# Performance work log

Measured on AMD Instinct MI355X. Metric: run time of the kernel, lower is better.

## Reference

```python
import jax, jax.numpy as jnp
import numpy as np

B, N, DIN, DOUT = 8, 2048, 512, 512
EDGE_P = 0.01  # edge probability for the random binary adjacency


def setup_inputs() -> dict:
    key = jax.random.key(0)
    k1, k2, k3, k4 = jax.random.split(key, 4)
    inputs = jax.random.normal(k1, (B, N, DIN), dtype=jnp.float32)
    # binary dense adjacency (dense_to_sparse discards weights -> edges are adj != 0)
    adj = (jax.random.uniform(k2, (B, N, N)) < EDGE_P).astype(jnp.float32)
    W = jax.random.normal(k3, (DIN, DOUT), dtype=jnp.float32) / np.sqrt(DIN)
    b = jax.random.normal(k4, (DOUT,), dtype=jnp.float32) * 0.01
    return {"inputs": inputs, "adj": adj, "W": W, "b": b}


def _gcn_norm(adj):
    # binary edge mask (edge weights from dense_to_sparse are discarded)
    A = (adj != 0).astype(adj.dtype)
    # add remaining self-loops: force diagonal to 1
    eye = jnp.eye(A.shape[-1], dtype=A.dtype)
    A = jnp.maximum(A, eye)
    deg = A.sum(axis=-1)                       # [B, N]
    dinv = jnp.where(deg > 0, jax.lax.rsqrt(deg), 0.0)
    # D^-1/2 (A + I) D^-1/2
    return dinv[..., :, None] * A * dinv[..., None, :]


def reference(inputs, adj, W, b):
    norm = _gcn_norm(adj)                      # [B, N, N]
    h = jnp.einsum('bnf,fo->bno', inputs, W)   # linear (no internal bias)
    agg = jnp.einsum('bnm,bmo->bno', norm, h)  # degree-normalized aggregation
    return jnp.tanh(agg + b)
```

## Files before the change

### kernel.cpp

```cpp
#include <hip/hip_runtime.h>
#include <hip/hip_bf16.h>
#include <math.h>


#define NROWS 16384
#define NCOLS 2048
#define DF    512
#define CAP   64

typedef __attribute__((ext_vector_type(8))) short bf16x8;
typedef __attribute__((ext_vector_type(4))) float f32x4;

typedef const void __attribute__((address_space(1))) gvoid_t;
typedef void __attribute__((address_space(3))) svoid_t;

__global__ __launch_bounds__(256) void convert_kernel(
    const float* __restrict__ X, const float* __restrict__ W,
    __hip_bfloat16* __restrict__ Xb, __hip_bfloat16* __restrict__ WT) {
  __shared__ float t[64][65];
  const int bid = blockIdx.x;
  const int tid = threadIdx.x;
  if (bid < 8192) {
    const int idx = bid * 256 + tid;
    const float4 v = ((const float4*)X)[idx];
    union { ushort4 u; __hip_bfloat16 h[4]; } p;
    p.h[0] = __float2bfloat16(v.x);
    p.h[1] = __float2bfloat16(v.y);
    p.h[2] = __float2bfloat16(v.z);
    p.h[3] = __float2bfloat16(v.w);
    ((ushort4*)Xb)[idx] = p.u;
  } else {
    const int b2 = bid - 8192;
    const int bx = b2 & 7, by = b2 >> 3;
    const int tx = tid & 63, ty = tid >> 6;
    #pragma unroll
    for (int i = 0; i < 16; ++i)
      t[ty + i * 4][tx] = W[(size_t)(by * 64 + ty + i * 4) * DF + bx * 64 + tx];
    __syncthreads();
    #pragma unroll
    for (int i = 0; i < 16; ++i)
      WT[(size_t)(bx * 64 + ty + i * 4) * DF + by * 64 + tx] =
          __float2bfloat16(t[tx][ty + i * 4]);
  }
}

__global__ __launch_bounds__(256) void build_edges(
    const float* __restrict__ adj, int* __restrict__ cnt,
    int* __restrict__ edges, float* __restrict__ dinv) {
  const int wave = threadIdx.x >> 6;
  const int lane = threadIdx.x & 63;
  const int r = blockIdx.x * 4 + wave;
  const int n = r & (NCOLS - 1);
  const float4* row4 = (const float4*)(adj + (size_t)r * NCOLS);
  const unsigned long long lt = (1ull << lane) - 1ull;
  int base = 0;
  for (int k = 0; k < NCOLS / 256; ++k) {
    const float4 v = row4[k * 64 + lane];
    const int c0 = k * 256 + lane * 4;
    const bool f0 = (v.x != 0.0f) || (c0 + 0 == n);
    const bool f1 = (v.y != 0.0f) || (c0 + 1 == n);
    const bool f2 = (v.z != 0.0f) || (c0 + 2 == n);
    const bool f3 = (v.w != 0.0f) || (c0 + 3 == n);
    const unsigned long long m0 = __ballot(f0);
    const unsigned long long m1 = __ballot(f1);
    const unsigned long long m2 = __ballot(f2);
    const unsigned long long m3 = __ballot(f3);
    const int n0 = __popcll(m0), n1 = __popcll(m1), n2 = __popcll(m2), n3 = __popcll(m3);
    if (f0) { int p = base + __popcll(m0 & lt);                 if (p < CAP) edges[(size_t)r * CAP + p] = c0 + 0; }
    if (f1) { int p = base + n0 + __popcll(m1 & lt);            if (p < CAP) edges[(size_t)r * CAP + p] = c0 + 1; }
    if (f2) { int p = base + n0 + n1 + __popcll(m2 & lt);       if (p < CAP) edges[(size_t)r * CAP + p] = c0 + 2; }
    if (f3) { int p = base + n0 + n1 + n2 + __popcll(m3 & lt);  if (p < CAP) edges[(size_t)r * CAP + p] = c0 + 3; }
    base += n0 + n1 + n2 + n3;
  }
  if (lane == 0) {
    cnt[r] = base < CAP ? base : CAP;
    dinv[r] = rsqrtf((float)base);
  }
}

__global__ __launch_bounds__(256) void gemm_bf16(
    const __hip_bfloat16* __restrict__ A, const __hip_bfloat16* __restrict__ BT,
    __hip_bfloat16* __restrict__ H) {
  __shared__ __hip_bfloat16 As[128 * 32];
  __shared__ __hip_bfloat16 Bs[128 * 32];
  const int tid = threadIdx.x;
  const int lane = tid & 63;
  const int w = tid >> 6;
  const int bm = blockIdx.y * 128;
  const int bn = blockIdx.x * 128;
  const int wm = (w >> 1) * 64;
  const int wn = (w & 1) * 64;

  f32x4 acc[4][4] = {};

  const int srow = tid >> 2;
  const int scol = (tid & 3) * 8;
  const int kl = (lane >> 4) * 8;
  const int rl = lane & 15;

  for (int k0 = 0; k0 < DF; k0 += 32) {
    #pragma unroll
    for (int i = 0; i < 2; ++i) {
      const __hip_bfloat16* ga = A + (size_t)(bm + i * 64 + srow) * DF + k0 + scol;
      const __hip_bfloat16* gb = BT + (size_t)(bn + i * 64 + srow) * DF + k0 + scol;
      char* la = (char*)As + i * 4096 + w * 1024;
      char* lb = (char*)Bs + i * 4096 + w * 1024;
      __builtin_amdgcn_global_load_lds((gvoid_t*)ga, (svoid_t*)la, 16, 0, 0);
      __builtin_amdgcn_global_load_lds((gvoid_t*)gb, (svoid_t*)lb, 16, 0, 0);
    }
    __syncthreads();

    bf16x8 af[4], bf[4];
    #pragma unroll
    for (int mi = 0; mi < 4; ++mi)
      af[mi] = *(const bf16x8*)&As[(wm + mi * 16 + rl) * 32 + kl];
    #pragma unroll
    for (int ni = 0; ni < 4; ++ni)
      bf[ni] = *(const bf16x8*)&Bs[(wn + ni * 16 + rl) * 32 + kl];
    #pragma unroll
    for (int mi = 0; mi < 4; ++mi)
      #pragma unroll
      for (int ni = 0; ni < 4; ++ni)
        acc[mi][ni] = __builtin_amdgcn_mfma_f32_16x16x32_bf16(af[mi], bf[ni], acc[mi][ni], 0, 0, 0);
    __syncthreads();
  }

  const int rq = (lane >> 4) * 4;
  #pragma unroll
  for (int mi = 0; mi < 4; ++mi)
    #pragma unroll
    for (int ni = 0; ni < 4; ++ni) {
      const int col = bn + wn + ni * 16 + rl;
      #pragma unroll
      for (int j = 0; j < 4; ++j) {
        const int row = bm + wm + mi * 16 + rq + j;
        H[(size_t)row * DF + col] = __float2bfloat16(acc[mi][ni][j]);
      }
    }
}

__global__ __launch_bounds__(256) void aggregate(
    const __hip_bfloat16* __restrict__ h, const int* __restrict__ cnt,
    const int* __restrict__ edges, const float* __restrict__ dinv,
    const float* __restrict__ bias, float* __restrict__ out) {
  __shared__ int   eL[CAP];
  __shared__ float wL[CAP];
  const int j = blockIdx.x;
  const int r = (j & 7) * NCOLS + (j >> 3);
  const int b = r >> 11;
  const int tid = threadIdx.x;
  const int c = cnt[r];
  if (tid < c) {
    const int m = edges[(size_t)r * CAP + tid];
    eL[tid] = m;
    wL[tid] = dinv[(b << 11) + m];
  }
  __syncthreads();

  float ax = 0.0f, ay = 0.0f;
  for (int e = 0; e < c; ++e) {
    const int m = eL[e];
    const float wgt = wL[e];
    const unsigned hv = *(const unsigned*)&h[((size_t)(b << 11) + m) * DF + tid * 2];
    ax += wgt * __uint_as_float(hv << 16);
    ay += wgt * __uint_as_float(hv & 0xffff0000u);
  }
  const float dn = dinv[r];
  const float2 bv = *(const float2*)&bias[tid * 2];
  float2 o;
  o.x = tanhf(ax * dn + bv.x);
  o.y = tanhf(ay * dn + bv.y);
  *(float2*)&out[(size_t)r * DF + tid * 2] = o;
}

extern "C" void kernel_launch(void* const* d_in, const int* in_sizes, int n_in,
                              void* d_out, int out_size, void* d_ws, size_t ws_size,
                              hipStream_t stream) {
  const float* X    = (const float*)d_in[0];
  const float* adj  = (const float*)d_in[1];
  const float* W    = (const float*)d_in[2];
  const float* bias = (const float*)d_in[3];
  float* out = (float*)d_out;

  char* ws = (char*)d_ws;
  __hip_bfloat16* Xb   = (__hip_bfloat16*)(ws);
  __hip_bfloat16* WT   = (__hip_bfloat16*)(ws + 16777216);
  __hip_bfloat16* h    = (__hip_bfloat16*)(ws + 17301504);
  float*          dinv = (float*)(ws + 34078720);
  int*            cnt  = (int*)  (ws + 34144256);
  int*            edges= (int*)  (ws + 34209792);

  convert_kernel<<<8256, 256, 0, stream>>>(X, W, Xb, WT);
  build_edges<<<NROWS / 4, 256, 0, stream>>>(adj, cnt, edges, dinv);
  gemm_bf16<<<dim3(4, 128), 256, 0, stream>>>(Xb, WT, h);
  aggregate<<<NROWS, 256, 0, stream>>>(h, cnt, edges, dinv, bias, out);
}
```

Baseline: 82.59 us.

## Fuse X conversion into GEMM, co-schedule edge build, wave-per-row aggregation

Drops the separate X-to-bf16 conversion pass: the GEMM now loads fp32 X directly, converts it in registers and writes the tile to LDS. The GEMM and the adjacency edge-list build are merged into one launch, so the compute-bound GEMM blocks can overlap with the bandwidth-bound adjacency scan. The GEMM tiles are remapped so that row tiles are grouped per XCD. Aggregation now assigns one wave per row with 16-byte loads and shuffle-broadcast edges, which removes the LDS staging and the barrier. The cost is that the A tile now goes through synchronous register loads instead of direct-to-LDS loads.

Result: slower. 87.78 us (+6.3%).

```diff
diff --git a/kernel.cpp b/kernel.cpp
--- a/kernel.cpp
+++ b/kernel.cpp
@@ -14,163 +14,181 @@
 typedef const void __attribute__((address_space(1))) gvoid_t;
 typedef void __attribute__((address_space(3))) svoid_t;
 
-__global__ __launch_bounds__(256) void convert_kernel(
-    const float* __restrict__ X, const float* __restrict__ W,
-    __hip_bfloat16* __restrict__ Xb, __hip_bfloat16* __restrict__ WT) {
+__global__ __launch_bounds__(256) void wt_kernel(
+    const float* __restrict__ W, __hip_bfloat16* __restrict__ WT) {
   __shared__ float t[64][65];
-  const int bid = blockIdx.x;
+  const int b2 = blockIdx.x;
+  const int bx = b2 & 7, by = b2 >> 3;
   const int tid = threadIdx.x;
-  if (bid < 8192) {
-    const int idx = bid * 256 + tid;
-    const float4 v = ((const float4*)X)[idx];
-    union { ushort4 u; __hip_bfloat16 h[4]; } p;
-    p.h[0] = __float2bfloat16(v.x);
-    p.h[1] = __float2bfloat16(v.y);
-    p.h[2] = __float2bfloat16(v.z);
-    p.h[3] = __float2bfloat16(v.w);
-    ((ushort4*)Xb)[idx] = p.u;
-  } else {
-    const int b2 = bid - 8192;
-    const int bx = b2 & 7, by = b2 >> 3;
-    const int tx = tid & 63, ty = tid >> 6;
-    #pragma unroll
-    for (int i = 0; i < 16; ++i)
-      t[ty + i * 4][tx] = W[(size_t)(by * 64 + ty + i * 4) * DF + bx * 64 + tx];
-    __syncthreads();
-    #pragma unroll
-    for (int i = 0; i < 16; ++i)
-      WT[(size_t)(bx * 64 + ty + i * 4) * DF + by * 64 + tx] =
-          __float2bfloat16(t[tx][ty + i * 4]);
-  }
-}
-
-__global__ __launch_bounds__(256) void build_edges(
-    const float* __restrict__ adj, int* __restrict__ cnt,
-    int* __restrict__ edges, float* __restrict__ dinv) {
-  const int wave = threadIdx.x >> 6;
-  const int lane = threadIdx.x & 63;
-  const int r = blockIdx.x * 4 + wave;
-  const int n = r & (NCOLS - 1);
-  const float4* row4 = (const float4*)(adj + (size_t)r * NCOLS);
-  const unsigned long long lt = (1ull << lane) - 1ull;
-  int base = 0;
-  for (int k = 0; k < NCOLS / 256; ++k) {
-    const float4 v = row4[k * 64 + lane];
-    const int c0 = k * 256 + lane * 4;
-    const bool f0 = (v.x != 0.0f) || (c0 + 0 == n);
-    const bool f1 = (v.y != 0.0f) || (c0 + 1 == n);
-    const bool f2 = (v.z != 0.0f) || (c0 + 2 == n);
-    const bool f3 = (v.w != 0.0f) || (c0 + 3 == n);
-    const unsigned long long m0 = __ballot(f0);
-    const unsigned long long m1 = __ballot(f1);
-    const unsigned long long m2 = __ballot(f2);
-    const unsigned long long m3 = __ballot(f3);
-    const int n0 = __popcll(m0), n1 = __popcll(m1), n2 = __popcll(m2), n3 = __popcll(m3);
-    if (f0) { int p = base + __popcll(m0 & lt);                 if (p < CAP) edges[(size_t)r * CAP + p] = c0 + 0; }
-    if (f1) { int p = base + n0 + __popcll(m1 & lt);            if (p < CAP) edges[(size_t)r * CAP + p] = c0 + 1; }
-    if (f2) { int p = base + n0 + n1 + __popcll(m2 & lt);       if (p < CAP) edges[(size_t)r * CAP + p] = c0 + 2; }
-    if (f3) { int p = base + n0 + n1 + n2 + __popcll(m3 & lt);  if (p < CAP) edges[(size_t)r * CAP + p] = c0 + 3; }
-    base += n0 + n1 + n2 + n3;
-  }
-  if (lane == 0) {
-    cnt[r] = base < CAP ? base : CAP;
-    dinv[r] = rsqrtf((float)base);
-  }
-}
-
-__global__ __launch_bounds__(256) void gemm_bf16(
-    const __hip_bfloat16* __restrict__ A, const __hip_bfloat16* __restrict__ BT,
-    __hip_bfloat16* __restrict__ H) {
+  const int tx = tid & 63, ty = tid >> 6;
+  #pragma unroll
+  for (int i = 0; i < 16; ++i)
+    t[ty + i * 4][tx] = W[(size_t)(by * 64 + ty + i * 4) * DF + bx * 64 + tx];
+  __syncthreads();
+  #pragma unroll
+  for (int i = 0; i < 16; ++i)
+    WT[(size_t)(bx * 64 + ty + i * 4) * DF + by * 64 + tx] =
+        __float2bfloat16(t[tx][ty + i * 4]);
+}
+
+__global__ __launch_bounds__(256) void fused_k1(
+    const float* __restrict__ X, const __hip_bfloat16* __restrict__ WT,
+    const float* __restrict__ adj, __hip_bfloat16* __restrict__ H,
+    int* __restrict__ cnt, int* __restrict__ edges, float* __restrict__ dinv) {
   __shared__ __hip_bfloat16 As[128 * 32];
   __shared__ __hip_bfloat16 Bs[128 * 32];
+  const int id = blockIdx.x;
   const int tid = threadIdx.x;
   const int lane = tid & 63;
   const int w = tid >> 6;
-  const int bm = blockIdx.y * 128;
-  const int bn = blockIdx.x * 128;
-  const int wm = (w >> 1) * 64;
-  const int wn = (w & 1) * 64;
-
-  f32x4 acc[4][4] = {};
-
-  const int srow = tid >> 2;
-  const int scol = (tid & 3) * 8;
-  const int kl = (lane >> 4) * 8;
-  const int rl = lane & 15;
-
-  for (int k0 = 0; k0 < DF; k0 += 32) {
-    #pragma unroll
-    for (int i = 0; i < 2; ++i) {
-      const __hip_bfloat16* ga = A + (size_t)(bm + i * 64 + srow) * DF + k0 + scol;
-      const __hip_bfloat16* gb = BT + (size_t)(bn + i * 64 + srow) * DF + k0 + scol;
-      char* la = (char*)As + i * 4096 + w * 1024;
-      char* lb = (char*)Bs + i * 4096 + w * 1024;
-      __builtin_amdgcn_global_load_lds((gvoid_t*)ga, (svoid_t*)la, 16, 0, 0);
-      __builtin_amdgcn_global_load_lds((gvoid_t*)gb, (svoid_t*)lb, 16, 0, 0);
+
+  if (id < 512) {
+    const int xcd = id & 7;
+    const int jj = id >> 3;
+    const int p  = xcd * 16 + (jj >> 2);
+    const int bm = p * 128;
+    const int bn = (jj & 3) * 128;
+
+    const int wm = (w >> 1) * 64;
+    const int wn = (w & 1) * 64;
+    const int srow = tid >> 2;
+    const int scol = (tid & 3) * 8;
+    const int arow = tid >> 1;
+    const int akh  = (tid & 1) * 16;
+    const int kl = (lane >> 4) * 8;
+    const int rl = lane & 15;
+
+    f32x4 acc[4][4] = {};
+
+    for (int k0 = 0; k0 < DF; k0 += 32) {
+      #pragma unroll
+      for (int i = 0; i < 2; ++i) {
+        const __hip_bfloat16* gb = WT + (size_t)(bn + i * 64 + srow) * DF + k0 + scol;
+        char* lb = (char*)Bs + i * 4096 + w * 1024;
+        __builtin_amdgcn_global_load_lds((gvoid_t*)gb, (svoid_t*)lb, 16, 0, 0);
+      }
+      const float* gaf = X + (size_t)(bm + arow) * DF + k0 + akh;
+      float xs[16];
+      *(float4*)&xs[0]  = ((const float4*)gaf)[0];
+      *(float4*)&xs[4]  = ((const float4*)gaf)[1];
+      *(float4*)&xs[8]  = ((const float4*)gaf)[2];
+      *(float4*)&xs[12] = ((const float4*)gaf)[3];
+      union { __hip_bfloat16 h[16]; uint4 q[2]; } pk;
+      #pragma unroll
+      for (int i = 0; i < 16; ++i) pk.h[i] = __float2bfloat16(xs[i]);
+      char* la = (char*)As + arow * 64 + akh * 2;
+      ((uint4*)la)[0] = pk.q[0];
+      ((uint4*)la)[1] = pk.q[1];
+
+      __syncthreads();
+
+      bf16x8 af[4], bf[4];
+      #pragma unroll
+      for (int mi = 0; mi < 4; ++mi)
+        af[mi] = *(const bf16x8*)&As[(wm + mi * 16 + rl) * 32 + kl];
+      #pragma unroll
+      for (int ni = 0; ni < 4; ++ni)
+        bf[ni] = *(const bf16x8*)&Bs[(wn + ni * 16 + rl) * 32 + kl];
+      #pragma unroll
+      for (int mi = 0; mi < 4; ++mi)
+        #pragma unroll
+        for (int ni = 0; ni < 4; ++ni)
+          acc[mi][ni] = __builtin_amdgcn_mfma_f32_16x16x32_bf16(af[mi], bf[ni], acc[mi][ni], 0, 0, 0);
+      __syncthreads();
     }
-    __syncthreads();
-
-    bf16x8 af[4], bf[4];
+
+    const int rq = (lane >> 4) * 4;
     #pragma unroll
     for (int mi = 0; mi < 4; ++mi)
-      af[mi] = *(const bf16x8*)&As[(wm + mi * 16 + rl) * 32 + kl];
+      #pragma unroll
+      for (int ni = 0; ni < 4; ++ni) {
+        const int col = bn + wn + ni * 16 + rl;
+        #pragma unroll
+        for (int j = 0; j < 4; ++j) {
+          const int row = bm + wm + mi * 16 + rq + j;
+          H[(size_t)row * DF + col] = __float2bfloat16(acc[mi][ni][j]);
+        }
+      }
+  } else {
+    const int r = (id - 512) * 4 + w;
+    const int n = r & (NCOLS - 1);
+    const float4* row4 = (const float4*)(adj + (size_t)r * NCOLS);
+    const unsigned long long lt = (1ull << lane) - 1ull;
+    int base = 0;
     #pragma unroll
-    for (int ni = 0; ni < 4; ++ni)
-      bf[ni] = *(const bf16x8*)&Bs[(wn + ni * 16 + rl) * 32 + kl];
-    #pragma unroll
-    for (int mi = 0; mi < 4; ++mi)
-      #pragma unroll
-      for (int ni = 0; ni < 4; ++ni)
-        acc[mi][ni] = __builtin_amdgcn_mfma_f32_16x16x32_bf16(af[mi], bf[ni], acc[mi][ni], 0, 0, 0);
-    __syncthreads();
+    for (int k = 0; k < NCOLS / 256; ++k) {
+      const float4 v = row4[k * 64 + lane];
+      const int c0 = k * 256 + lane * 4;
+      const bool f0 = (v.x != 0.0f) || (c0 + 0 == n);
+      const bool f1 = (v.y != 0.0f) || (c0 + 1 == n);
+      const bool f2 = (v.z != 0.0f) || (c0 + 2 == n);
+      const bool f3 = (v.w != 0.0f) || (c0 + 3 == n);
+      const unsigned long long m0 = __ballot(f0);
+      const unsigned long long m1 = __ballot(f1);
+      const unsigned long long m2 = __ballot(f2);
+      const unsigned long long m3 = __ballot(f3);
+      const int n0 = __popcll(m0), n1 = __popcll(m1), n2 = __popcll(m2), n3 = __popcll(m3);
+      if (f0) { int p = base + __popcll(m0 & lt);                if (p < CAP) edges[(size_t)r * CAP + p] = c0 + 0; }
+      if (f1) { int p = base + n0 + __popcll(m1 & lt);           if (p < CAP) edges[(size_t)r * CAP + p] = c0 + 1; }
+      if (f2) { int p = base + n0 + n1 + __popcll(m2 & lt);      if (p < CAP) edges[(size_t)r * CAP + p] = c0 + 2; }
+      if (f3) { int p = base + n0 + n1 + n2 + __popcll(m3 & lt); if (p < CAP) edges[(size_t)r * CAP + p] = c0 + 3; }
+      base += n0 + n1 + n2 + n3;
+    }
+    if (lane == 0) {
+      cnt[r] = base < CAP ? base : CAP;
+      dinv[r] = rsqrtf((float)base);
+    }
   }
-
-  const int rq = (lane >> 4) * 4;
-  #pragma unroll
-  for (int mi = 0; mi < 4; ++mi)
-    #pragma unroll
-    for (int ni = 0; ni < 4; ++ni) {
-      const int col = bn + wn + ni * 16 + rl;
-      #pragma unroll
-      for (int j = 0; j < 4; ++j) {
-        const int row = bm + wm + mi * 16 + rq + j;
-        H[(size_t)row * DF + col] = __float2bfloat16(acc[mi][ni][j]);
-      }
-    }
 }
 
 __global__ __launch_bounds__(256) void aggregate(
     const __hip_bfloat16* __restrict__ h, const int* __restrict__ cnt,
     const int* __restrict__ edges, const float* __restrict__ dinv,
     const float* __restrict__ bias, float* __restrict__ out) {
-  __shared__ int   eL[CAP];
-  __shared__ float wL[CAP];
-  const int j = blockIdx.x;
+  const int lane = threadIdx.x & 63;
+  const int wv = threadIdx.x >> 6;
+  const int j = blockIdx.x * 4 + wv;
   const int r = (j & 7) * NCOLS + (j >> 3);
   const int b = r >> 11;
-  const int tid = threadIdx.x;
   const int c = cnt[r];
-  if (tid < c) {
-    const int m = edges[(size_t)r * CAP + tid];
-    eL[tid] = m;
-    wL[tid] = dinv[(b << 11) + m];
+  int   ml = 0;
+  float wl = 0.0f;
+  if (lane < c) {
+    ml = edges[(size_t)r * CAP + lane];
+    wl = dinv[(b << 11) + ml];
   }
-  __syncthreads();
-
-  float ax = 0.0f, ay = 0.0f;
+  const float4* b4 = (const float4*)bias;
+  const float4 bb0 = b4[lane * 2];
+  const float4 bb1 = b4[lane * 2 + 1];
+
+  float acc[8] = {0.f, 0.f, 0.f, 0.f, 0.f, 0.f, 0.f, 0.f};
+  const uint4* hbase = (const uint4*)(h + ((size_t)(b << 11)) * DF);
   for (int e = 0; e < c; ++e) {
-    const int m = eL[e];
-    const float wgt = wL[e];
-    const unsigned hv = *(const unsigned*)&h[((size_t)(b << 11) + m) * DF + tid * 2];
-    ax += wgt * __uint_as_float(hv << 16);
-    ay += wgt * __uint_as_float(hv & 0xffff0000u);
+    const int   m  = __shfl(ml, e);
+    const float wt = __shfl(wl, e);
+    const uint4 hv = hbase[(size_t)m * 64 + lane];
+    acc[0] += wt * __uint_as_float(hv.x << 16);
+    acc[1] += wt * __uint_as_float(hv.x & 0xffff0000u);
+    acc[2] += wt * __uint_as_float(hv.y << 16);
+    acc[3] += wt * __uint_as_float(hv.y & 0xffff0000u);
+    acc[4] += wt * __uint_as_float(hv.z << 16);
+    acc[5] += wt * __uint_as_float(hv.z & 0xffff0000u);
+    acc[6] += wt * __uint_as_float(hv.w << 16);
+    acc[7] += wt * __uint_as_float(hv.w & 0xffff0000u);
   }
   const float dn = dinv[r];
-  const float2 bv = *(const float2*)&bias[tid * 2];
-  float2 o;
-  o.x = tanhf(ax * dn + bv.x);
-  o.y = tanhf(ay * dn + bv.y);
-  *(float2*)&out[(size_t)r * DF + tid * 2] = o;
+  float4 o0, o1;
+  o0.x = tanhf(acc[0] * dn + bb0.x);
+  o0.y = tanhf(acc[1] * dn + bb0.y);
+  o0.z = tanhf(acc[2] * dn + bb0.z);
+  o0.w = tanhf(acc[3] * dn + bb0.w);
+  o1.x = tanhf(acc[4] * dn + bb1.x);
+  o1.y = tanhf(acc[5] * dn + bb1.y);
+  o1.z = tanhf(acc[6] * dn + bb1.z);
+  o1.w = tanhf(acc[7] * dn + bb1.w);
+  float4* op = (float4*)(out + (size_t)r * DF + lane * 8);
+  op[0] = o0;
+  op[1] = o1;
 }
 
 extern "C" void kernel_launch(void* const* d_in, const int* in_sizes, int n_in,
@@ -183,15 +201,13 @@
   float* out = (float*)d_out;
 
   char* ws = (char*)d_ws;
-  __hip_bfloat16* Xb   = (__hip_bfloat16*)(ws);
+  __hip_bfloat16* h    = (__hip_bfloat16*)(ws);
   __hip_bfloat16* WT   = (__hip_bfloat16*)(ws + 16777216);
-  __hip_bfloat16* h    = (__hip_bfloat16*)(ws + 17301504);
-  float*          dinv = (float*)(ws + 34078720);
-  int*            cnt  = (int*)  (ws + 34144256);
-  int*            edges= (int*)  (ws + 34209792);
-
-  convert_kernel<<<8256, 256, 0, stream>>>(X, W, Xb, WT);
-  build_edges<<<NROWS / 4, 256, 0, stream>>>(adj, cnt, edges, dinv);
-  gemm_bf16<<<dim3(4, 128), 256, 0, stream>>>(Xb, WT, h);
-  aggregate<<<NROWS, 256, 0, stream>>>(h, cnt, edges, dinv, bias, out);
-}
+  float*          dinv = (float*)(ws + 17301504);
+  int*            cnt  = (int*)  (ws + 17367040);
+  int*            edges= (int*)  (ws + 17432576);
+
+  wt_kernel<<<64, 256, 0, stream>>>(W, WT);
+  fused_k1<<<512 + NROWS / 4, 256, 0, stream>>>(X, WT, adj, h, cnt, edges, dinv);
+  aggregate<<<NROWS / 4, 256, 0, stream>>>(h, cnt, edges, dinv, bias, out);
+}
```
